# Kernel tuning notes

Hardware: AMD Instinct MI355X
Metric: run time of the kernel (lower is better)

The kernel has to match this reference:

```python
import jax, jax.numpy as jnp
import numpy as np

EPS = 1e-8  # F.cosine_similarity eps


def _cosine(nb, q):
    # nb: [N1, k, d], q: [N1, d] -> [N1, k]
    dot = jnp.einsum('nkd,nd->nk', nb, q)
    nb_norm = jnp.maximum(jnp.linalg.norm(nb, axis=-1), EPS)
    q_norm = jnp.maximum(jnp.linalg.norm(q, axis=-1), EPS)[:, None]
    return dot / (nb_norm * q_norm)


def setup_inputs() -> dict:
    key = jax.random.key(0)
    k0, k1, k2, k3 = jax.random.split(key, 4)
    N1, N2, D = 2048, 50000, 512
    return {
        'query_emb0': jax.random.normal(k0, (N1, D), dtype=jnp.float32),
        'query_emb1': jax.random.normal(k1, (N1, D), dtype=jnp.float32),
        'cand_emb0': jax.random.normal(k2, (N2, D), dtype=jnp.float32),
        'cand_emb1': jax.random.normal(k3, (N2, D), dtype=jnp.float32),
        'k': 32,
    }


def reference(query_emb0, query_emb1, cand_emb0, cand_emb1, k):
    # --- get_KNN_batch: L2 cdist on the ORIGINAL embeddings only (matches torch) ---
    # ||q - c||^2 = ||q||^2 + ||c||^2 - 2 q.c  (GEMM-based, compute-bound)
    q2 = jnp.sum(query_emb0 * query_emb0, axis=1, keepdims=True)       # [N1,1]
    c2 = jnp.sum(cand_emb0 * cand_emb0, axis=1)[None, :]               # [1,N2]
    d2 = jnp.maximum(q2 + c2 - 2.0 * (query_emb0 @ cand_emb0.T), 0.0)  # [N1,N2]
    dist = jnp.sqrt(d2)
    # topk of -distance == k nearest
    _, top_k_idx = jax.lax.top_k(-dist, k)                             # [N1,k]

    # --- get_neighbor_embeddings: gather both tables ---
    nb0 = cand_emb0[top_k_idx]  # [N1,k,d]
    nb1 = cand_emb1[top_k_idx]  # [N1,k,d]

    # --- compute_cosine_batch: elementwise max of the two cosine tables ---
    cos0 = _cosine(nb0, query_emb0)
    cos1 = _cosine(nb1, query_emb1)
    cosine_table = jnp.where(cos0 > cos1, cos0, cos1)                  # [N1,k]
    return cosine_table, jnp.mean(cosine_table, axis=-1)
```

## Files before the change

### kernel.cpp

```cpp
#include <hip/hip_runtime.h>
#include <math.h>


#define D       512
#define KSEL    32
#define NSELMX  64
#define NCF     8
#define TOPL    5
#define CEPS    1e-8f
#define INF     __builtin_inff()

#define MTF     32
#define NTF     256
#define KCF     64
#define NTHF    256

#define MT      64
#define NT      512
#define KC      64
#define NTH     512

using s16x8  = __attribute__((ext_vector_type(8)))  short;
using f32x16 = __attribute__((ext_vector_type(16))) float;

__device__ __forceinline__ void async16(const void* g, void* s) {
  __builtin_amdgcn_global_load_lds(
      (const __attribute__((address_space(1))) unsigned int*)g,
      (__attribute__((address_space(3))) unsigned int*)s, 16, 0, 0);
}

__device__ __forceinline__ unsigned int bfhi2(float x0, float x1) {
  unsigned int u0 = __float_as_uint(x0), u1 = __float_as_uint(x1);
  u0 = (u0 + 0x7fffu + ((u0 >> 16) & 1u)) >> 16;
  u1 = (u1 + 0x7fffu + ((u1 >> 16) & 1u)) & 0xffff0000u;
  return u0 | u1;
}

__global__ __launch_bounds__(256) void sumsq_cvt_kernel(
    const float* __restrict__ C, const float* __restrict__ Q,
    float* __restrict__ c2, float* __restrict__ q2,
    unsigned short* __restrict__ Cb, unsigned short* __restrict__ Qb,
    int n2, int n1)
{
  int wid  = threadIdx.x >> 6;
  int lane = threadIdx.x & 63;
  int row  = blockIdx.x * 4 + wid;
  const float* src; float* dst; unsigned short* bdst;
  if (row < n2) { src = C + (size_t)row * D; dst = c2 + row; bdst = Cb + (size_t)row * D; }
  else {
    int r = row - n2; if (r >= n1) return;
    src = Q + (size_t)r * D; dst = q2 + r; bdst = Qb + (size_t)r * D;
  }
  const float4* s4 = (const float4*)src;
  float4 a = s4[2*lane], b = s4[2*lane + 1];
  float s = a.x*a.x + a.y*a.y + a.z*a.z + a.w*a.w
          + b.x*b.x + b.y*b.y + b.z*b.z + b.w*b.w;
  int4 h;
  h.x = (int)bfhi2(a.x, a.y); h.y = (int)bfhi2(a.z, a.w);
  h.z = (int)bfhi2(b.x, b.y); h.w = (int)bfhi2(b.z, b.w);
  *(int4*)(bdst + 8*lane) = h;
  #pragma unroll
  for (int o = 32; o > 0; o >>= 1) s += __shfl_down(s, o, 64);
  if (lane == 0) *dst = s;
}

__global__ __launch_bounds__(256) void rows_sumsq_kernel(
    const float* __restrict__ C, const float* __restrict__ Q,
    float* __restrict__ c2, float* __restrict__ q2, int n2, int n1)
{
  int wid  = threadIdx.x >> 6;
  int lane = threadIdx.x & 63;
  int row  = blockIdx.x * 4 + wid;
  const float* src; float* dst;
  if (row < n2) { src = C + (size_t)row * D; dst = c2 + row; }
  else { int r = row - n2; if (r >= n1) return; src = Q + (size_t)r * D; dst = q2 + r; }
  const float4* s4 = (const float4*)src;
  float4 a = s4[lane], b = s4[lane + 64];
  float s = a.x*a.x + a.y*a.y + a.z*a.z + a.w*a.w
          + b.x*b.x + b.y*b.y + b.z*b.z + b.w*b.w;
  #pragma unroll
  for (int o = 32; o > 0; o >>= 1) s += __shfl_down(s, o, 64);
  if (lane == 0) *dst = s;
}

__device__ inline void worst_reduce(float dIn, int iIn, float& wd, int& wi) {
  float dd = dIn; int ii = iIn;
  #pragma unroll
  for (int o = 1; o <= 16; o <<= 1) {
    float dp = __shfl_xor(dd, o, 64);
    int   ip = __shfl_xor(ii, o, 64);
    bool take = (dp > dd) || (dp == dd && ip > ii);
    dd = take ? dp : dd; ii = take ? ip : ii;
  }
  wd = __shfl(dd, 0, 64); wi = __shfl(ii, 0, 64);
}

__device__ inline void cvt8(const float4 a, const float4 b, int4& hi, int4& lo) {
  float x[8] = {a.x, a.y, a.z, a.w, b.x, b.y, b.z, b.w};
  unsigned int hw[8], lw[8];
  #pragma unroll
  for (int j = 0; j < 8; ++j) {
    unsigned int ux = __float_as_uint(x[j]);
    unsigned int rh = (ux + 0x7fffu + ((ux >> 16) & 1u)) & 0xffff0000u;
    float rl = x[j] - __uint_as_float(rh);
    unsigned int ul = __float_as_uint(rl);
    hw[j] = rh >> 16;
    lw[j] = (ul + 0x7fffu + ((ul >> 16) & 1u)) >> 16;
  }
  hi = make_int4((int)(hw[0]|(hw[1]<<16)), (int)(hw[2]|(hw[3]<<16)),
                 (int)(hw[4]|(hw[5]<<16)), (int)(hw[6]|(hw[7]<<16)));
  lo = make_int4((int)(lw[0]|(lw[1]<<16)), (int)(lw[2]|(lw[3]<<16)),
                 (int)(lw[4]|(lw[5]<<16)), (int)(lw[6]|(lw[7]<<16)));
}

__global__ __launch_bounds__(NTHF, 2) void knn_phase1_bf_kernel(
    const unsigned short* __restrict__ Qb, const unsigned short* __restrict__ Cb,
    const float* __restrict__ q2g, const float* __restrict__ c2g,
    float* __restrict__ tkd, int* __restrict__ tki,
    int n1, int n2, int chunk, int nc)
{
  extern __shared__ char smem[];
  unsigned short* ch = (unsigned short*)smem;
  float* dl = (float*)(smem + 65536);

  const int tid  = threadIdx.x;
  const int w    = tid >> 6;
  const int l    = tid & 63;
  const int l31  = l & 31;
  const int half = l >> 5;
  const int bid     = blockIdx.x;
  const int chunkid = bid & (NCF - 1);
  const int mbase   = (bid >> 3) * MTF;
  const int cbase0  = chunkid * chunk;
  const int cend    = min(cbase0 + chunk, n2);

  float q2w[8];
  #pragma unroll
  for (int g = 0; g < 8; ++g)
    q2w[g] = q2g[min(mbase + 8*(g>>1) + 2*w + (g&1), n1 - 1)];

  s16x8 qreg[8][4];
  {
    int gm = min(mbase + l31, n1 - 1);
    const unsigned short* qrow = Qb + (size_t)gm * D + half*8;
    #pragma unroll
    for (int kb = 0; kb < 8; ++kb)
      #pragma unroll
      for (int ks = 0; ks < 4; ++ks)
        qreg[kb][ks] = *(const s16x8*)(qrow + kb*64 + ks*16);
  }

  unsigned long long vv[8][TOPL];
  #pragma unroll
  for (int g = 0; g < 8; ++g)
    #pragma unroll
    for (int t = 0; t < TOPL; ++t) vv[g][t] = 0xffffffffffffffffULL;

  const int lrow = l >> 3;
  const int su   = (l & 7) ^ lrow;

  auto STAGE = [&](int buf, int kb, int cb) {
    #pragma unroll
    for (int i = 0; i < 8; ++i) {
      int gn = cb + w*64 + i*8 + lrow;
      const unsigned short* src = Cb + (size_t)gn * D + kb*KCF + su*8;
      unsigned short* dst = ch + buf*(256*64) + (w*64 + i*8)*64;
      async16(src, dst);
    }
  };

  f32x16 zf;
  #pragma unroll
  for (int e = 0; e < 16; ++e) zf[e] = 0.f;

  const int nsteps = (cend - cbase0 + NTF - 1) / NTF;
  int b = 0;
  STAGE(0, 0, cbase0);
  __syncthreads();

  for (int nt = 0; nt < nsteps; ++nt) {
    const int cbase = cbase0 + nt * NTF;
    f32x16 acc[2];
    acc[0] = zf; acc[1] = zf;

    #pragma unroll
    for (int kb = 0; kb < 8; ++kb) {
      if (kb + 1 < 8) {
        STAGE(b^1, kb+1, cbase);
        asm volatile("s_waitcnt vmcnt(8)" ::: "memory");
      } else if (nt + 1 < nsteps) {
        STAGE(b^1, 0, cbase + NTF);
        asm volatile("s_waitcnt vmcnt(8)" ::: "memory");
      } else {
        asm volatile("s_waitcnt vmcnt(0)" ::: "memory");
      }
      __builtin_amdgcn_s_barrier();
      __builtin_amdgcn_sched_barrier(0);

      const unsigned short* cbf = ch + b*(256*64);
      #pragma unroll
      for (int ks = 0; ks < 4; ++ks) {
        const int u = 2*ks + half;
        s16x8 cf[2];
        #pragma unroll
        for (int ct = 0; ct < 2; ++ct) {
          int c = w*64 + ct*32 + l31;
          cf[ct] = *(const s16x8*)(cbf + c*64 + (u ^ (c & 7))*8);
        }
        acc[0] = __builtin_amdgcn_mfma_f32_32x32x16_bf16(qreg[kb][ks], cf[0], acc[0], 0, 0, 0);
        acc[1] = __builtin_amdgcn_mfma_f32_32x32x16_bf16(qreg[kb][ks], cf[1], acc[1], 0, 0, 0);
      }
      asm volatile("s_waitcnt lgkmcnt(0)" ::: "memory");
      __builtin_amdgcn_s_barrier();
      __builtin_amdgcn_sched_barrier(0);
      b ^= 1;
    }

    float c2v[2]; int vld[2];
    #pragma unroll
    for (int ct = 0; ct < 2; ++ct) {
      int gc = cbase + w*64 + ct*32 + l31;
      vld[ct] = (gc < cend);
      c2v[ct] = vld[ct] ? c2g[gc] : 0.f;
    }
    #pragma unroll
    for (int p = 0; p < 4; ++p) {
      #pragma unroll
      for (int jj = 0; jj < 4; ++jj)
        #pragma unroll
        for (int ct = 0; ct < 2; ++ct) {
          float a = acc[ct][4*p + jj];
          float s = c2v[ct] - 2.f * a;
          dl[(4*half + jj)*NTF + w*64 + ct*32 + l31] = vld[ct] ? s : INF;
        }
      __syncthreads();
      #pragma unroll
      for (int s2 = 0; s2 < 2; ++s2) {
        const int g = 2*p + s2;
        const float q2u = q2w[g];
        float4 sv4 = *((const float4*)(dl + (2*w + s2)*NTF) + l);
        float svs[4] = {sv4.x, sv4.y, sv4.z, sv4.w};
        #pragma unroll
        for (int jj = 0; jj < 4; ++jj) {
          float d2v = fmaxf(q2u + svs[jj], 0.f);
          unsigned int kbit = __float_as_uint(d2v);
          unsigned int ci = (kbit != 0x7f800000u) ? (unsigned)(cbase + 4*l + jj)
                                                  : 0x7fffffffu;
          unsigned long long e = ((unsigned long long)kbit << 32) | ci;
          if (e < vv[g][TOPL-1]) {
            vv[g][TOPL-1] = e;
            #pragma unroll
            for (int t = TOPL-1; t > 0; --t) {
              unsigned long long lo = vv[g][t-1] < vv[g][t] ? vv[g][t-1] : vv[g][t];
              unsigned long long hi = vv[g][t-1] < vv[g][t] ? vv[g][t]   : vv[g][t-1];
              vv[g][t-1] = lo; vv[g][t] = hi;
            }
          }
        }
      }
      __syncthreads();
    }
  }

  unsigned long long* sel = (unsigned long long*)smem + (size_t)w * 2048;
  const unsigned long long mlt = (l == 0) ? 0ull : ((~0ull) >> (64 - l));
  __syncthreads();
  #pragma unroll
  for (int g = 0; g < 8; ++g) {
    unsigned int pk = (unsigned int)(vv[g][0] >> 32);
    #pragma unroll
    for (int o = 1; o < 64; o <<= 1) {
      unsigned int other = (unsigned int)__shfl_xor((int)pk, o, 64);
      pk = (other > pk) ? other : pk;
    }
    int cnt = 0;
    #pragma unroll
    for (int t = 0; t < TOPL; ++t) cnt += ((unsigned int)(vv[g][t] >> 32) <= pk) ? 1 : 0;
    unsigned long long b0 = __ballot(cnt & 1);
    unsigned long long b1 = __ballot(cnt & 2);
    unsigned long long b2 = __ballot(cnt & 4);
    int pre = __popcll(b0 & mlt) + 2*__popcll(b1 & mlt) + 4*__popcll(b2 & mlt);
    int Ns  = __popcll(b0) + 2*__popcll(b1) + 4*__popcll(b2);
    #pragma unroll
    for (int t = 0; t < TOPL; ++t)
      if (t < cnt) sel[pre + t] = vv[g][t];
    asm volatile("s_waitcnt lgkmcnt(0)" ::: "memory");
    __builtin_amdgcn_sched_barrier(0);
    int rk[TOPL];
    #pragma unroll
    for (int t = 0; t < TOPL; ++t) rk[t] = 0;
    for (int j = 0; j < Ns; ++j) {
      unsigned long long e = sel[j];
      #pragma unroll
      for (int t = 0; t < TOPL; ++t) rk[t] += (e < vv[g][t]) ? 1 : 0;
    }
    int gq = mbase + 8*(g>>1) + 2*w + (g&1);
    if (gq < n1) {
      #pragma unroll
      for (int t = 0; t < TOPL; ++t)
        if (t < cnt && rk[t] < KSEL) {
          size_t o = ((size_t)gq * nc + chunkid) * KSEL + rk[t];
          tkd[o] = __uint_as_float((unsigned int)(vv[g][t] >> 32));
          tki[o] = (int)(unsigned int)(vv[g][t] & 0xffffffffu);
        }
    }
  }
}

__global__ __launch_bounds__(NTH) void knn_phase1_cvt_kernel(
    const float* __restrict__ Q, const float* __restrict__ C,
    const float* __restrict__ q2g, const float* __restrict__ c2g,
    float* __restrict__ tkd, int* __restrict__ tki,
    int n1, int n2, int chunk, int nc)
{
  extern __shared__ char smem[];
  unsigned short* qh = (unsigned short*)smem;
  unsigned short* ql = qh + 64*64;
  unsigned short* ch = ql + 64*64;
  unsigned short* cl = ch + 512*64;
  float* dl = (float*)(smem + 147456);

  const int tid  = threadIdx.x;
  const int w    = tid >> 6;
  const int l    = tid & 63;
  const int l31  = l & 31;
  const int half = l >> 5;
  const int mbase   = blockIdx.x * MT;
  const int chunkid = blockIdx.y;
  const int cbase0  = chunkid * chunk;
  const int cend    = min(cbase0 + chunk, n2);

  float q2w[8];
  #pragma unroll
  for (int g = 0; g < 8; ++g) q2w[g] = q2g[min(mbase + g*8 + w, n1 - 1)];

  float listd[8]; int listi[8]; float wd4[8]; int wi4[8];
  #pragma unroll
  for (int g = 0; g < 8; ++g) { listd[g]=INF; listi[g]=0x7fffffff; wd4[g]=INF; wi4[g]=0x7fffffff; }

  const int srow = tid >> 3;
  const int sk8  = (tid & 7) * 8;
  const int su   = (tid & 7);

  float4 cva[8][2], qva[2];
  auto LOADR = [&](int kb, int cb) {
    {
      int gr = min(mbase + srow, n1 - 1);
      const float4* p = (const float4*)(Q + (size_t)gr * D + kb*KC + sk8);
      qva[0] = p[0]; qva[1] = p[1];
    }
    #pragma unroll
    for (int r = 0; r < 8; ++r) {
      int gn = cb + srow + 64*r;
      if (gn < cend) {
        const float4* p = (const float4*)(C + (size_t)gn * D + kb*KC + sk8);
        cva[r][0] = p[0]; cva[r][1] = p[1];
      } else {
        cva[r][0] = make_float4(0.f,0.f,0.f,0.f);
        cva[r][1] = make_float4(0.f,0.f,0.f,0.f);
      }
    }
  };
  auto STORE = [&]() {
    int4 hi, lo;
    {
      int idx = srow*64 + (su ^ (srow & 7))*8;
      cvt8(qva[0], qva[1], hi, lo);
      *(int4*)(qh + idx) = hi; *(int4*)(ql + idx) = lo;
    }
    #pragma unroll
    for (int r = 0; r < 8; ++r) {
      int row = srow + 64*r;
      int idx = row*64 + (su ^ (row & 7))*8;
      cvt8(cva[r][0], cva[r][1], hi, lo);
      *(int4*)(ch + idx) = hi; *(int4*)(cl + idx) = lo;
    }
  };

  f32x16 zf;
  #pragma unroll
  for (int e = 0; e < 16; ++e) zf[e] = 0.f;

  const int nsteps = (cend - cbase0 + NT - 1) / NT;
  LOADR(0, cbase0);

  for (int nt = 0; nt < nsteps; ++nt) {
    const int cbase = cbase0 + nt * NT;
    f32x16 acc[2][2];
    #pragma unroll
    for (int rt = 0; rt < 2; ++rt)
      #pragma unroll
      for (int ct = 0; ct < 2; ++ct) acc[rt][ct] = zf;

    for (int kb = 0; kb < D/KC; ++kb) {
      __syncthreads();
      STORE();
      __syncthreads();
      if (kb + 1 < D/KC)        LOADR(kb + 1, cbase);
      else if (nt + 1 < nsteps) LOADR(0, cbase + NT);

      #pragma unroll
      for (int ks = 0; ks < 4; ++ks) {
        const int u = 2*ks + half;
        s16x8 qf[2][2], cf[2][2];
        #pragma unroll
        for (int rt = 0; rt < 2; ++rt) {
          int r = rt*32 + l31;
          int idx = r*64 + (u ^ (r & 7))*8;
          qf[rt][0] = *(const s16x8*)(qh + idx);
          qf[rt][1] = *(const s16x8*)(ql + idx);
        }
        #pragma unroll
        for (int ct = 0; ct < 2; ++ct) {
          int c = w*64 + ct*32 + l31;
          int idx = c*64 + (u ^ (c & 7))*8;
          cf[ct][0] = *(const s16x8*)(ch + idx);
          cf[ct][1] = *(const s16x8*)(cl + idx);
        }
        #pragma unroll
        for (int rt = 0; rt < 2; ++rt)
          #pragma unroll
          for (int ct = 0; ct < 2; ++ct) {
            acc[rt][ct] = __builtin_amdgcn_mfma_f32_32x32x16_bf16(qf[rt][0], cf[ct][0], acc[rt][ct], 0, 0, 0);
            acc[rt][ct] = __builtin_amdgcn_mfma_f32_32x32x16_bf16(qf[rt][0], cf[ct][1], acc[rt][ct], 0, 0, 0);
            acc[rt][ct] = __builtin_amdgcn_mfma_f32_32x32x16_bf16(qf[rt][1], cf[ct][0], acc[rt][ct], 0, 0, 0);
          }
      }
    }

    float c2v[2]; int vld[2];
    #pragma unroll
    for (int ct = 0; ct < 2; ++ct) {
      int gc = cbase + w*64 + ct*32 + l31;
      vld[ct] = (gc < cend);
      c2v[ct] = vld[ct] ? c2g[gc] : 0.f;
    }
    #pragma unroll
    for (int g = 0; g < 8; ++g) {
      const int rt = g >> 2, qq = g & 3;
      #pragma unroll
      for (int jj = 0; jj < 4; ++jj)
        #pragma unroll
        for (int ct = 0; ct < 2; ++ct) {
          float a = acc[rt][ct][4*qq + jj];
          float s = c2v[ct] - 2.f * a;
          dl[(4*half + jj)*512 + w*64 + ct*32 + l31] = vld[ct] ? s : INF;
        }
      __syncthreads();
      const float q2u = q2w[g];
      #pragma unroll
      for (int j2 = 0; j2 < 8; ++j2) {
        float sv = dl[w*512 + l + 64*j2];
        float dv = sqrtf(fmaxf(q2u + sv, 0.f));
        unsigned long long mask = __ballot(dv < wd4[g]);
        while (mask) {
          int L = __ffsll(mask) - 1; mask &= mask - 1;
          float dnew = __shfl(dv, L, 64);
          int ci = cbase + 64*j2 + L;
          if ((dnew < wd4[g]) || (dnew == wd4[g] && ci < wi4[g])) {
            bool isw = (l < 32) && (listd[g] == wd4[g]) && (listi[g] == wi4[g]);
            int wl = __ffsll(__ballot(isw)) - 1;
            if (l == wl) { listd[g] = dnew; listi[g] = ci; }
            worst_reduce((l < 32) ? listd[g] : -1.f,
                         (l < 32) ? listi[g] : -1, wd4[g], wi4[g]);
          }
        }
      }
      __syncthreads();
    }
  }

  #pragma unroll
  for (int g = 0; g < 8; ++g) {
    int gq = mbase + g*8 + w;
    float d = listd[g]; int i = listi[g];
    int rank = 0;
    #pragma unroll
    for (int j = 0; j < KSEL; ++j) {
      float dj = __shfl(listd[g], j, 64);
      int   ij = __shfl(listi[g], j, 64);
      rank += (dj < d) || (dj == d && ij < i);
    }
    if (l < 32 && gq < n1) {
      size_t o = ((size_t)gq * nc + chunkid) * KSEL + rank;
      tkd[o] = d; tki[o] = i;
    }
  }
}

__global__ __launch_bounds__(256) void knn_phase2_kernel(
    const float* __restrict__ Q0, const float* __restrict__ Q1,
    const float* __restrict__ C0, const float* __restrict__ C1,
    const float* __restrict__ q2g, const float* __restrict__ c2g,
    const float* __restrict__ tkd, const int* __restrict__ tki,
    float* __restrict__ out, int n1, int n2, int nc)
{
  __shared__ float q0s[D], q1s[D];
  __shared__ float pd[256]; __shared__ int pi[256];
  __shared__ float nd[NSELMX]; __shared__ int ni[NSELMX];
  __shared__ float de[NSELMX];
  __shared__ int   fi[KSEL];
  __shared__ float cosj[KSEL];
  __shared__ float red0[4], red1[4], qn[2];

  const int q = blockIdx.x, tid = threadIdx.x;
  const int npool = nc * KSEL;
  const int nsel  = (NSELMX < npool) ? NSELMX : npool;

  if (tid < 128) ((float4*)q0s)[tid] = ((const float4*)(Q0 + (size_t)q*D))[tid];
  else           ((float4*)q1s)[tid-128] = ((const float4*)(Q1 + (size_t)q*D))[tid-128];
  if (tid < npool) { pd[tid] = tkd[(size_t)q*npool + tid]; pi[tid] = tki[(size_t)q*npool + tid]; }
  __syncthreads();

  float a0 = q0s[tid], b0 = q0s[tid+256], a1 = q1s[tid], b1 = q1s[tid+256];
  float s0 = a0*a0 + b0*b0, s1 = a1*a1 + b1*b1;
  #pragma unroll
  for (int o = 32; o > 0; o >>= 1) { s0 += __shfl_down(s0, o, 64); s1 += __shfl_down(s1, o, 64); }
  int lane = tid & 63, wid = tid >> 6;
  if (lane == 0) { red0[wid] = s0; red1[wid] = s1; }

  if (tid < npool) {
    float dm = pd[tid]; int im = pi[tid]; int rank = 0;
    for (int j = 0; j < npool; ++j) {
      float dj = pd[j]; int ij = pi[j];
      rank += (dj < dm) || (dj == dm && ij < im);
    }
    if (rank < nsel) { nd[rank] = dm; ni[rank] = im; }
  }
  __syncthreads();
  if (tid == 0) {
    qn[0] = fmaxf(sqrtf(red0[0]+red0[1]+red0[2]+red0[3]), CEPS);
    qn[1] = fmaxf(sqrtf(red1[0]+red1[1]+red1[2]+red1[3]), CEPS);
  }

  const float q2q = q2g[q];
  const int ll = tid & 7;
  for (int base = 0; base < NSELMX; base += 32) {
    int g = base + (tid >> 3);
    if (g < nsel) {
      int ix = ni[g];
      bool okx = (ix >= 0 && ix < n2);
      int ixc = okx ? ix : 0;
      const float4* r0  = (const float4*)(C0 + (size_t)ixc * D);
      const float4* q04 = (const float4*)q0s;
      float dot = 0.f;
      #pragma unroll
      for (int r = 0; r < 16; ++r) {
        float4 v = r0[r*8 + ll], u = q04[r*8 + ll];
        dot = fmaf(v.x,u.x, fmaf(v.y,u.y, fmaf(v.z,u.z, fmaf(v.w,u.w, dot))));
      }
      #pragma unroll
      for (int o = 4; o > 0; o >>= 1) dot += __shfl_xor(dot, o, 64);
      if (ll == 0) de[g] = okx ? sqrtf(fmaxf(q2q + c2g[ixc] - 2.f*dot, 0.f)) : INF;
    }
  }
  __syncthreads();

  if (tid < nsel) {
    float dm = de[tid]; int im = ni[tid]; int rank = 0;
    for (int j = 0; j < nsel; ++j) {
      float dj = de[j]; int ij = ni[j];
      rank += (dj < dm) || (dj == dm && ij < im);
    }
    if (rank < KSEL) fi[rank] = im;
  }
  __syncthreads();

  const int g = tid >> 3;
  int ix = fi[g];
  ix = (ix >= 0 && ix < n2) ? ix : 0;
  const float4* r0  = (const float4*)(C0 + (size_t)ix * D);
  const float4* r1  = (const float4*)(C1 + (size_t)ix * D);
  const float4* q04 = (const float4*)q0s;
  const float4* q14 = (const float4*)q1s;
  float dot0 = 0.f, nn0 = 0.f, dot1 = 0.f, nn1 = 0.f;
  #pragma unroll
  for (int r = 0; r < 16; ++r) {
    int e4 = r*8 + ll;
    float4 v0 = r0[e4], qv0 = q04[e4];
    dot0 = fmaf(v0.x,qv0.x, fmaf(v0.y,qv0.y, fmaf(v0.z,qv0.z, fmaf(v0.w,qv0.w, dot0))));
    nn0  = fmaf(v0.x,v0.x,  fmaf(v0.y,v0.y,  fmaf(v0.z,v0.z,  fmaf(v0.w,v0.w,  nn0))));
    float4 v1 = r1[e4], qv1 = q14[e4];
    dot1 = fmaf(v1.x,qv1.x, fmaf(v1.y,qv1.y, fmaf(v1.z,qv1.z, fmaf(v1.w,qv1.w, dot1))));
    nn1  = fmaf(v1.x,v1.x,  fmaf(v1.y,v1.y,  fmaf(v1.z,v1.z,  fmaf(v1.w,v1.w,  nn1))));
  }
  #pragma unroll
  for (int o = 4; o > 0; o >>= 1) {
    dot0 += __shfl_xor(dot0, o, 64); nn0 += __shfl_xor(nn0, o, 64);
    dot1 += __shfl_xor(dot1, o, 64); nn1 += __shfl_xor(nn1, o, 64);
  }
  if (ll == 0) {
    float c0 = dot0 / (fmaxf(sqrtf(nn0), CEPS) * qn[0]);
    float c1 = dot1 / (fmaxf(sqrtf(nn1), CEPS) * qn[1]);
    float cv = (c0 > c1) ? c0 : c1;
    out[(size_t)q * KSEL + g] = cv;
    cosj[g] = cv;
  }
  __syncthreads();
  if (tid == 0) {
    float s = 0.f;
    #pragma unroll
    for (int j = 0; j < KSEL; ++j) s += cosj[j];
    out[(size_t)n1 * KSEL + q] = s * (1.f / KSEL);
  }
}

extern "C" void kernel_launch(void* const* d_in, const int* in_sizes, int n_in,
                              void* d_out, int out_size, void* d_ws, size_t ws_size,
                              hipStream_t stream)
{
  const float* Q0 = (const float*)d_in[0];
  const float* Q1 = (const float*)d_in[1];
  const float* C0 = (const float*)d_in[2];
  const float* C1 = (const float*)d_in[3];
  const int n1 = in_sizes[0] / D;
  const int n2 = in_sizes[2] / D;
  float* out = (float*)d_out;
  if (n1 <= 0 || n2 <= 0) return;

  char* wsb = (char*)d_ws;
  size_t c2n = ((size_t)n2 + 127) & ~(size_t)127;
  size_t q2n = ((size_t)n1 + 127) & ~(size_t)127;

  size_t off_c2  = 0;
  size_t off_q2  = off_c2 + c2n*4;
  size_t off_tkd = off_q2 + q2n*4;
  size_t off_tki = off_tkd + (size_t)n1*NCF*KSEL*4;
  size_t off_cb  = (off_tki + (size_t)n1*NCF*KSEL*4 + 255) & ~(size_t)255;
  size_t off_qb  = off_cb + ((size_t)n2 + 512)*D*2;
  size_t need    = off_qb + (size_t)n1*D*2;
  bool fast = (ws_size >= need);

  if (fast) {
    float* c2  = (float*)(wsb + off_c2);
    float* q2  = (float*)(wsb + off_q2);
    float* tkd = (float*)(wsb + off_tkd);
    int*   tki = (int*)(wsb + off_tki);
    unsigned short* Cb = (unsigned short*)(wsb + off_cb);
    unsigned short* Qb = (unsigned short*)(wsb + off_qb);

    sumsq_cvt_kernel<<<(n2 + n1 + 3)/4, 256, 0, stream>>>(C0, Q0, c2, q2, Cb, Qb, n2, n1);

    const int chunk  = (n2 + NCF - 1) / NCF;
    const int mtiles = (n1 + MTF - 1) / MTF;
    (void)hipFuncSetAttribute((const void*)knn_phase1_bf_kernel,
                              hipFuncAttributeMaxDynamicSharedMemorySize, 73728);
    knn_phase1_bf_kernel<<<mtiles * NCF, NTHF, 73728, stream>>>(
        Qb, Cb, q2, c2, tkd, tki, n1, n2, chunk, NCF);
    knn_phase2_kernel<<<n1, 256, 0, stream>>>(Q0, Q1, C0, C1, q2, c2, tkd, tki, out, n1, n2, NCF);
  } else {
    float* wsf = (float*)d_ws;
    int nc = 8;
    while (nc > 1 && (c2n + q2n + (size_t)n1 * nc * KSEL * 2) * 4 > ws_size) nc >>= 1;
    float* c2  = wsf;
    float* q2  = wsf + c2n;
    float* tkd = wsf + c2n + q2n;
    int*   tki = (int*)(wsf + c2n + q2n + (size_t)n1 * nc * KSEL);

    rows_sumsq_kernel<<<(n2 + n1 + 3)/4, 256, 0, stream>>>(C0, Q0, c2, q2, n2, n1);
    const int chunk  = (n2 + nc - 1) / nc;
    const int mtiles = (n1 + MT - 1) / MT;
    (void)hipFuncSetAttribute((const void*)knn_phase1_cvt_kernel,
                              hipFuncAttributeMaxDynamicSharedMemorySize, 163840);
    knn_phase1_cvt_kernel<<<dim3(mtiles, nc), NTH, 163840, stream>>>(
        Q0, C0, q2, c2, tkd, tki, n1, n2, chunk, nc);
    knn_phase2_kernel<<<n1, 256, 0, stream>>>(Q0, Q1, C0, C1, q2, c2, tkd, tki, out, n1, n2, nc);
  }
}
```

Measured before the change: 492.8 us.

## Restructure distance GEMM pipeline: per-wave staging, streamed Q fragments, no block barriers

The first-pass distance GEMM no longer keeps all 32 Q fragments in registers. It streams them per K-block into two alternating register sets, which frees VGPRs. Candidate staging becomes a two-deep prefetch with precomputed incrementing source pointers and precomputed swizzled LDS offsets. The per-K-block s_barrier pairs are dropped, relying on each wave loading and consuming only its own 64 candidate rows, and s_setprio is raised around the MFMA section. This removes synchronization and register pressure, but correctness now depends on the wave-private LDS layout and on vmcnt accounting, including the extra Q global loads counted in vmcnt.

```diff
diff --git a/kernel.cpp b/kernel.cpp
--- a/kernel.cpp
+++ b/kernel.cpp
@@ -28,6 +28,10 @@
       (const __attribute__((address_space(1))) unsigned int*)g,
       (__attribute__((address_space(3))) unsigned int*)s, 16, 0, 0);
 }
+
+#define BARL() do { asm volatile("s_waitcnt lgkmcnt(0)" ::: "memory"); \
+                    __builtin_amdgcn_s_barrier();                      \
+                    asm volatile("" ::: "memory"); } while (0)
 
 __device__ __forceinline__ unsigned int bfhi2(float x0, float x1) {
   unsigned int u0 = __float_as_uint(x0), u1 = __float_as_uint(x1);
@@ -139,17 +143,6 @@
   for (int g = 0; g < 8; ++g)
     q2w[g] = q2g[min(mbase + 8*(g>>1) + 2*w + (g&1), n1 - 1)];
 
-  s16x8 qreg[8][4];
-  {
-    int gm = min(mbase + l31, n1 - 1);
-    const unsigned short* qrow = Qb + (size_t)gm * D + half*8;
-    #pragma unroll
-    for (int kb = 0; kb < 8; ++kb)
-      #pragma unroll
-      for (int ks = 0; ks < 4; ++ks)
-        qreg[kb][ks] = *(const s16x8*)(qrow + kb*64 + ks*16);
-  }
-
   unsigned long long vv[8][TOPL];
   #pragma unroll
   for (int g = 0; g < 8; ++g)
@@ -159,63 +152,50 @@
   const int lrow = l >> 3;
   const int su   = (l & 7) ^ lrow;
 
-  auto STAGE = [&](int buf, int kb, int cb) {
-    #pragma unroll
-    for (int i = 0; i < 8; ++i) {
-      int gn = cb + w*64 + i*8 + lrow;
-      const unsigned short* src = Cb + (size_t)gn * D + kb*KCF + su*8;
-      unsigned short* dst = ch + buf*(256*64) + (w*64 + i*8)*64;
-      async16(src, dst);
+  const unsigned short* qptr = Qb + (size_t)min(mbase + l31, n1 - 1) * D + half*8;
+  s16x8 qA[4], qB[4];
+  #pragma unroll
+  for (int ks = 0; ks < 4; ++ks) qA[ks] = *(const s16x8*)(qptr + ks*16);
+
+  const unsigned short* csrc[8];
+  #pragma unroll
+  for (int i = 0; i < 8; ++i)
+    csrc[i] = Cb + (size_t)(cbase0 + w*64 + i*8 + lrow) * D + su*8;
+  int ss = 0;
+
+  auto STAGEP = [&](int buf) {
+    unsigned short* db = ch + buf*(256*64) + (w*64)*64;
+    #pragma unroll
+    for (int i = 0; i < 8; ++i) { async16(csrc[i], db + i*8*64); csrc[i] += KCF; }
+    if (((++ss) & 7) == 0) {
+      #pragma unroll
+      for (int i = 0; i < 8; ++i) csrc[i] += (size_t)(NTF - 1) * D;
     }
   };
 
+  int coff[2][4];
+  #pragma unroll
+  for (int ct = 0; ct < 2; ++ct)
+    #pragma unroll
+    for (int ks = 0; ks < 4; ++ks) {
+      int c = w*64 + ct*32 + l31;
+      int u = 2*ks + half;
+      coff[ct][ks] = c*64 + (u ^ (c & 7))*8;
+    }
+
   f32x16 zf;
   #pragma unroll
   for (int e = 0; e < 16; ++e) zf[e] = 0.f;
 
   const int nsteps = (cend - cbase0 + NTF - 1) / NTF;
-  int b = 0;
-  STAGE(0, 0, cbase0);
-  __syncthreads();
+  STAGEP(0);
+  STAGEP(1);
 
   for (int nt = 0; nt < nsteps; ++nt) {
     const int cbase = cbase0 + nt * NTF;
     f32x16 acc[2];
     acc[0] = zf; acc[1] = zf;
 
-    #pragma unroll
-    for (int kb = 0; kb < 8; ++kb) {
-      if (kb + 1 < 8) {
-        STAGE(b^1, kb+1, cbase);
-        asm volatile("s_waitcnt vmcnt(8)" ::: "memory");
-      } else if (nt + 1 < nsteps) {
-        STAGE(b^1, 0, cbase + NTF);
-        asm volatile("s_waitcnt vmcnt(8)" ::: "memory");
-      } else {
-        asm volatile("s_waitcnt vmcnt(0)" ::: "memory");
-      }
-      __builtin_amdgcn_s_barrier();
-      __builtin_amdgcn_sched_barrier(0);
-
-      const unsigned short* cbf = ch + b*(256*64);
-      #pragma unroll
-      for (int ks = 0; ks < 4; ++ks) {
-        const int u = 2*ks + half;
-        s16x8 cf[2];
-        #pragma unroll
-        for (int ct = 0; ct < 2; ++ct) {
-          int c = w*64 + ct*32 + l31;
-          cf[ct] = *(const s16x8*)(cbf + c*64 + (u ^ (c & 7))*8);
-        }
-        acc[0] = __builtin_amdgcn_mfma_f32_32x32x16_bf16(qreg[kb][ks], cf[0], acc[0], 0, 0, 0);
-        acc[1] = __builtin_amdgcn_mfma_f32_32x32x16_bf16(qreg[kb][ks], cf[1], acc[1], 0, 0, 0);
-      }
-      asm volatile("s_waitcnt lgkmcnt(0)" ::: "memory");
-      __builtin_amdgcn_s_barrier();
-      __builtin_amdgcn_sched_barrier(0);
-      b ^= 1;
-    }
-
     float c2v[2]; int vld[2];
     #pragma unroll
     for (int ct = 0; ct < 2; ++ct) {
@@ -223,6 +203,45 @@
       vld[ct] = (gc < cend);
       c2v[ct] = vld[ct] ? c2g[gc] : 0.f;
     }
+
+    #pragma unroll
+    for (int kb = 0; kb < 8; ++kb) {
+      if (nt == nsteps - 1 && kb == 7)
+        asm volatile("s_waitcnt vmcnt(0)" ::: "memory");
+      else
+        asm volatile("s_waitcnt vmcnt(8)" ::: "memory");
+
+      {
+        const int kbn = (kb + 1) & 7;
+        if ((kb & 1) == 0) {
+          #pragma unroll
+          for (int ks = 0; ks < 4; ++ks)
+            qB[ks] = *(const s16x8*)(qptr + kbn*64 + ks*16);
+        } else {
+          #pragma unroll
+          for (int ks = 0; ks < 4; ++ks)
+            qA[ks] = *(const s16x8*)(qptr + kbn*64 + ks*16);
+        }
+      }
+
+      const unsigned short* cbf = ch + (kb & 1)*(256*64);
+      __builtin_amdgcn_s_setprio(1);
+      #pragma unroll
+      for (int ks = 0; ks < 4; ++ks) {
+        s16x8 cf0 = *(const s16x8*)(cbf + coff[0][ks]);
+        s16x8 cf1 = *(const s16x8*)(cbf + coff[1][ks]);
+        s16x8 qv  = (kb & 1) ? qB[ks] : qA[ks];
+        acc[0] = __builtin_amdgcn_mfma_f32_32x32x16_bf16(qv, cf0, acc[0], 0, 0, 0);
+        acc[1] = __builtin_amdgcn_mfma_f32_32x32x16_bf16(qv, cf1, acc[1], 0, 0, 0);
+      }
+      __builtin_amdgcn_s_setprio(0);
+
+      if (nt < nsteps - 1 || kb < 6) {
+        asm volatile("s_waitcnt lgkmcnt(0)" ::: "memory");
+        STAGEP(kb & 1);
+      }
+    }
+
     #pragma unroll
     for (int p = 0; p < 4; ++p) {
       #pragma unroll
@@ -233,7 +252,7 @@
           float s = c2v[ct] - 2.f * a;
           dl[(4*half + jj)*NTF + w*64 + ct*32 + l31] = vld[ct] ? s : INF;
         }
-      __syncthreads();
+      BARL();
       #pragma unroll
       for (int s2 = 0; s2 < 2; ++s2) {
         const int g = 2*p + s2;
@@ -258,7 +277,7 @@
           }
         }
       }
-      __syncthreads();
+      BARL();
     }
   }
 
```

Result: slower. 533.1 us (+8.2%).

## Restructure bf16 KNN phase1 with 4-deep LDS ring, LDS-resident queries, 512 threads

Applied to the files above, without the earlier changes.

Rewrites the bf16 distance+top-k kernel so that query tiles live in swizzled LDS instead of registers. Candidate tiles now stream through a 4-slot ring of 32-wide K chunks, with per-wave waits and no block barrier per K step. Block size doubles to 512 threads, each wave owns 32 candidate columns and 4 query rows, and c2 is prefetched per tile. The goal is to cut register pressure and barrier stalls and deepen memory prefetch, at the cost of more LDS (128KB), which limits occupancy to one block per CU, plus more LDS reads for query fragments.

```diff
diff --git a/kernel.cpp b/kernel.cpp
--- a/kernel.cpp
+++ b/kernel.cpp
@@ -12,8 +12,8 @@
 
 #define MTF     32
 #define NTF     256
-#define KCF     64
-#define NTHF    256
+#define KCF     32
+#define NTHF    512
 
 #define MT      64
 #define NT      512
@@ -28,6 +28,10 @@
       (const __attribute__((address_space(1))) unsigned int*)g,
       (__attribute__((address_space(3))) unsigned int*)s, 16, 0, 0);
 }
+
+#define BARL() do { asm volatile("s_waitcnt lgkmcnt(0)" ::: "memory"); \
+                    __builtin_amdgcn_s_barrier();                      \
+                    asm volatile("" ::: "memory"); } while (0)
 
 __device__ __forceinline__ unsigned int bfhi2(float x0, float x1) {
   unsigned int u0 = __float_as_uint(x0), u1 = __float_as_uint(x1);
@@ -120,8 +124,9 @@
     int n1, int n2, int chunk, int nc)
 {
   extern __shared__ char smem[];
-  unsigned short* ch = (unsigned short*)smem;
-  float* dl = (float*)(smem + 65536);
+  unsigned short* qs = (unsigned short*)smem;
+  char* ringb = smem + 32768;
+  float* dl   = (float*)(smem + 98304);
 
   const int tid  = threadIdx.x;
   const int w    = tid >> 6;
@@ -134,37 +139,37 @@
   const int cbase0  = chunkid * chunk;
   const int cend    = min(cbase0 + chunk, n2);
 
-  float q2w[8];
-  #pragma unroll
-  for (int g = 0; g < 8; ++g)
-    q2w[g] = q2g[min(mbase + 8*(g>>1) + 2*w + (g&1), n1 - 1)];
-
-  s16x8 qreg[8][4];
-  {
-    int gm = min(mbase + l31, n1 - 1);
-    const unsigned short* qrow = Qb + (size_t)gm * D + half*8;
-    #pragma unroll
-    for (int kb = 0; kb < 8; ++kb)
-      #pragma unroll
-      for (int ks = 0; ks < 4; ++ks)
-        qreg[kb][ks] = *(const s16x8*)(qrow + kb*64 + ks*16);
-  }
-
-  unsigned long long vv[8][TOPL];
-  #pragma unroll
-  for (int g = 0; g < 8; ++g)
+  float q2w[4];
+  #pragma unroll
+  for (int g = 0; g < 4; ++g) q2w[g] = q2g[min(mbase + w*4 + g, n1 - 1)];
+
+  unsigned long long vv[4][TOPL];
+  #pragma unroll
+  for (int g = 0; g < 4; ++g)
     #pragma unroll
     for (int t = 0; t < TOPL; ++t) vv[g][t] = 0xffffffffffffffffULL;
 
-  const int lrow = l >> 3;
-  const int su   = (l & 7) ^ lrow;
-
-  auto STAGE = [&](int buf, int kb, int cb) {
-    #pragma unroll
-    for (int i = 0; i < 8; ++i) {
-      int gn = cb + w*64 + i*8 + lrow;
-      const unsigned short* src = Cb + (size_t)gn * D + kb*KCF + su*8;
-      unsigned short* dst = ch + buf*(256*64) + (w*64 + i*8)*64;
+  float4 c2cur = *(const float4*)(c2g + cbase0 + 4*l);
+  float4 c2nxt = c2cur;
+
+  #pragma unroll
+  for (int g = 0; g < 4; ++g) {
+    int rho = w*4 + g;
+    int gq  = min(mbase + rho, n1 - 1);
+    const unsigned short* src = Qb + (size_t)gq * D + (size_t)((l ^ (rho & 7)) * 8);
+    unsigned short* dst = qs + rho * 512;
+    async16(src, dst);
+  }
+
+  const int srcu = (l & 3) ^ ((l >> 3) & 3);
+  auto STAGE = [&](int slot, int s4) {
+    int t4 = s4 >> 4, kb4 = s4 & 15;
+    int rowg = cbase0 + t4*NTF + w*32;
+    #pragma unroll
+    for (int i = 0; i < 2; ++i) {
+      int gr = rowg + i*16 + (l >> 2);
+      const unsigned short* src = Cb + (size_t)gr * D + kb4*KCF + srcu*8;
+      unsigned short* dst = (unsigned short*)(ringb + slot*16384) + (w*32 + i*16)*32;
       async16(src, dst);
     }
   };
@@ -173,100 +178,89 @@
   #pragma unroll
   for (int e = 0; e < 16; ++e) zf[e] = 0.f;
 
-  const int nsteps = (cend - cbase0 + NTF - 1) / NTF;
-  int b = 0;
-  STAGE(0, 0, cbase0);
-  __syncthreads();
-
-  for (int nt = 0; nt < nsteps; ++nt) {
+  const int nst   = (cend - cbase0 + NTF - 1) / NTF;
+  const int total = nst * 16;
+  STAGE(0,0); STAGE(1,1); STAGE(2,2); STAGE(3,3);
+  asm volatile("s_waitcnt vmcnt(6)" ::: "memory");
+  __builtin_amdgcn_s_barrier();
+
+  const unsigned short* qrow = qs + l31 * 512;
+  f32x16 acc = zf;
+
+  for (int nt = 0; nt < nst; ++nt) {
     const int cbase = cbase0 + nt * NTF;
-    f32x16 acc[2];
-    acc[0] = zf; acc[1] = zf;
-
-    #pragma unroll
-    for (int kb = 0; kb < 8; ++kb) {
-      if (kb + 1 < 8) {
-        STAGE(b^1, kb+1, cbase);
-        asm volatile("s_waitcnt vmcnt(8)" ::: "memory");
-      } else if (nt + 1 < nsteps) {
-        STAGE(b^1, 0, cbase + NTF);
-        asm volatile("s_waitcnt vmcnt(8)" ::: "memory");
-      } else {
-        asm volatile("s_waitcnt vmcnt(0)" ::: "memory");
+
+    #pragma unroll
+    for (int kb = 0; kb < 16; ++kb) {
+      const int s   = nt*16 + kb;
+      const int rem = total - 1 - s;
+      if (rem > 2)       asm volatile("s_waitcnt vmcnt(6)" ::: "memory");
+      else if (rem == 2) asm volatile("s_waitcnt vmcnt(4)" ::: "memory");
+      else if (rem == 1) asm volatile("s_waitcnt vmcnt(2)" ::: "memory");
+      else               asm volatile("s_waitcnt vmcnt(0)" ::: "memory");
+
+      if (kb == 0)
+        c2nxt = *(const float4*)(c2g + cbase + NTF + 4*l);
+
+      const unsigned short* cb_ =
+          (const unsigned short*)(ringb + (s & 3)*16384) + (w*32 + l31)*32;
+      #pragma unroll
+      for (int ks = 0; ks < 2; ++ks) {
+        int qu = ((kb << 2) + (ks << 1) + half) ^ (l31 & 7);
+        s16x8 qf = *(const s16x8*)(qrow + qu*8);
+        int p  = ((ks << 1) + half) ^ ((l31 >> 1) & 3);
+        s16x8 cf = *(const s16x8*)(cb_ + p*8);
+        acc = __builtin_amdgcn_mfma_f32_32x32x16_bf16(qf, cf, acc, 0, 0, 0);
       }
-      __builtin_amdgcn_s_barrier();
-      __builtin_amdgcn_sched_barrier(0);
-
-      const unsigned short* cbf = ch + b*(256*64);
-      #pragma unroll
-      for (int ks = 0; ks < 4; ++ks) {
-        const int u = 2*ks + half;
-        s16x8 cf[2];
-        #pragma unroll
-        for (int ct = 0; ct < 2; ++ct) {
-          int c = w*64 + ct*32 + l31;
-          cf[ct] = *(const s16x8*)(cbf + c*64 + (u ^ (c & 7))*8);
-        }
-        acc[0] = __builtin_amdgcn_mfma_f32_32x32x16_bf16(qreg[kb][ks], cf[0], acc[0], 0, 0, 0);
-        acc[1] = __builtin_amdgcn_mfma_f32_32x32x16_bf16(qreg[kb][ks], cf[1], acc[1], 0, 0, 0);
+      if (s + 4 < total) {
+        asm volatile("s_waitcnt lgkmcnt(0)" ::: "memory");
+        STAGE(s & 3, s + 4);
       }
-      asm volatile("s_waitcnt lgkmcnt(0)" ::: "memory");
-      __builtin_amdgcn_s_barrier();
-      __builtin_amdgcn_sched_barrier(0);
-      b ^= 1;
-    }
-
-    float c2v[2]; int vld[2];
-    #pragma unroll
-    for (int ct = 0; ct < 2; ++ct) {
-      int gc = cbase + w*64 + ct*32 + l31;
-      vld[ct] = (gc < cend);
-      c2v[ct] = vld[ct] ? c2g[gc] : 0.f;
-    }
-    #pragma unroll
-    for (int p = 0; p < 4; ++p) {
-      #pragma unroll
-      for (int jj = 0; jj < 4; ++jj)
-        #pragma unroll
-        for (int ct = 0; ct < 2; ++ct) {
-          float a = acc[ct][4*p + jj];
-          float s = c2v[ct] - 2.f * a;
-          dl[(4*half + jj)*NTF + w*64 + ct*32 + l31] = vld[ct] ? s : INF;
-        }
-      __syncthreads();
-      #pragma unroll
-      for (int s2 = 0; s2 < 2; ++s2) {
-        const int g = 2*p + s2;
+    }
+
+    #pragma unroll
+    for (int r = 0; r < 16; ++r) {
+      int row = (r & 3) + 8*(r >> 2) + 4*half;
+      dl[row*NTF + w*32 + l31] = acc[r];
+    }
+    BARL();
+    {
+      float c2s[4] = {c2cur.x, c2cur.y, c2cur.z, c2cur.w};
+      #pragma unroll
+      for (int g = 0; g < 4; ++g) {
         const float q2u = q2w[g];
-        float4 sv4 = *((const float4*)(dl + (2*w + s2)*NTF) + l);
+        float4 sv4 = *((const float4*)(dl + (w*4 + g)*NTF) + l);
         float svs[4] = {sv4.x, sv4.y, sv4.z, sv4.w};
         #pragma unroll
         for (int jj = 0; jj < 4; ++jj) {
-          float d2v = fmaxf(q2u + svs[jj], 0.f);
-          unsigned int kbit = __float_as_uint(d2v);
-          unsigned int ci = (kbit != 0x7f800000u) ? (unsigned)(cbase + 4*l + jj)
-                                                  : 0x7fffffffu;
-          unsigned long long e = ((unsigned long long)kbit << 32) | ci;
-          if (e < vv[g][TOPL-1]) {
-            vv[g][TOPL-1] = e;
-            #pragma unroll
-            for (int t = TOPL-1; t > 0; --t) {
-              unsigned long long lo = vv[g][t-1] < vv[g][t] ? vv[g][t-1] : vv[g][t];
-              unsigned long long hi = vv[g][t-1] < vv[g][t] ? vv[g][t]   : vv[g][t-1];
-              vv[g][t-1] = lo; vv[g][t] = hi;
+          int ci = cbase + 4*l + jj;
+          if (ci < cend) {
+            float d2v = fmaxf(q2u + c2s[jj] - 2.f*svs[jj], 0.f);
+            unsigned long long e =
+                ((unsigned long long)__float_as_uint(d2v) << 32) | (unsigned int)ci;
+            if (e < vv[g][TOPL-1]) {
+              vv[g][TOPL-1] = e;
+              #pragma unroll
+              for (int t = TOPL-1; t > 0; --t) {
+                unsigned long long lo = vv[g][t-1] < vv[g][t] ? vv[g][t-1] : vv[g][t];
+                unsigned long long hi = vv[g][t-1] < vv[g][t] ? vv[g][t]   : vv[g][t-1];
+                vv[g][t-1] = lo; vv[g][t] = hi;
+              }
             }
           }
         }
       }
-      __syncthreads();
-    }
-  }
-
-  unsigned long long* sel = (unsigned long long*)smem + (size_t)w * 2048;
+    }
+    BARL();
+    acc = zf;
+    c2cur = c2nxt;
+  }
+
+  unsigned long long* sel = (unsigned long long*)smem + (size_t)w * 512;
   const unsigned long long mlt = (l == 0) ? 0ull : ((~0ull) >> (64 - l));
   __syncthreads();
   #pragma unroll
-  for (int g = 0; g < 8; ++g) {
+  for (int g = 0; g < 4; ++g) {
     unsigned int pk = (unsigned int)(vv[g][0] >> 32);
     #pragma unroll
     for (int o = 1; o < 64; o <<= 1) {
@@ -294,7 +288,7 @@
       #pragma unroll
       for (int t = 0; t < TOPL; ++t) rk[t] += (e < vv[g][t]) ? 1 : 0;
     }
-    int gq = mbase + 8*(g>>1) + 2*w + (g&1);
+    int gq = mbase + w*4 + g;
     if (gq < n1) {
       #pragma unroll
       for (int t = 0; t < TOPL; ++t)
@@ -644,8 +638,8 @@
     const int chunk  = (n2 + NCF - 1) / NCF;
     const int mtiles = (n1 + MTF - 1) / MTF;
     (void)hipFuncSetAttribute((const void*)knn_phase1_bf_kernel,
-                              hipFuncAttributeMaxDynamicSharedMemorySize, 73728);
-    knn_phase1_bf_kernel<<<mtiles * NCF, NTHF, 73728, stream>>>(
+                              hipFuncAttributeMaxDynamicSharedMemorySize, 131072);
+    knn_phase1_bf_kernel<<<mtiles * NCF, NTHF, 131072, stream>>>(
         Qb, Cb, q2, c2, tkd, tki, n1, n2, chunk, NCF);
     knn_phase2_kernel<<<n1, 256, 0, stream>>>(Q0, Q1, C0, C1, q2, c2, tkd, tki, out, n1, n2, NCF);
   } else {
```

Measured after the change: 540.9 us. 1.1x slower.
